# Kernel optimization log

Hardware: AMD Instinct MI355X
Metric: run time of the kernel (lower is better)

Reference implementation:

```python
import jax, jax.numpy as jnp
import numpy as np
jax.config.update("jax_enable_x64", True)

I_SIZE, H, L = 128, 512, 2
B, T = 64, 512


def setup_inputs() -> dict:
    key = jax.random.key(0)
    ks = jax.random.split(key, 9)
    bound = 1.0 / np.sqrt(H)  # PyTorch LSTM init: U(-1/sqrt(H), 1/sqrt(H))
    u = lambda k, shape: jax.random.uniform(k, shape, jnp.float64, -bound, bound)
    return {
        "x": jax.random.normal(ks[0], (B, T, I_SIZE), jnp.float32),
        "W_ih0": u(ks[1], (4 * H, I_SIZE)),
        "W_hh0": u(ks[2], (4 * H, H)),
        "b_ih0": u(ks[3], (4 * H,)),
        "b_hh0": u(ks[4], (4 * H,)),
        "W_ih1": u(ks[5], (4 * H, H)),
        "W_hh1": u(ks[6], (4 * H, H)),
        "b_ih1": u(ks[7], (4 * H,)),
        "b_hh1": u(ks[8], (4 * H,)),
        "h0": jnp.zeros((L, 1, H), jnp.float64),
        "c0": jnp.zeros((L, 1, H), jnp.float64),
    }


def _lstm_layer(x, W_ih, W_hh, b_ih, b_hh, h0, c0):
    # x: [B, T, in]; PyTorch gate order: i, f, g, o
    xg = jnp.einsum("bti,gi->btg", x, W_ih) + b_ih + b_hh  # [B, T, 4H]

    def step(carry, xg_t):
        h, c = carry
        gates = xg_t + h @ W_hh.T  # [B, 4H]
        i, f, g, o = jnp.split(gates, 4, axis=-1)
        c = jax.nn.sigmoid(f) * c + jax.nn.sigmoid(i) * jnp.tanh(g)
        h = jax.nn.sigmoid(o) * jnp.tanh(c)
        return (h, c), h

    (_, _), hs = jax.lax.scan(step, (h0, c0), jnp.swapaxes(xg, 0, 1))
    return jnp.swapaxes(hs, 0, 1)  # [B, T, H]


def reference(x, W_ih0, W_hh0, b_ih0, b_hh0, W_ih1, W_hh1, b_ih1, b_hh1, h0, c0):
    xd = x.astype(jnp.float64)
    b = xd.shape[0]
    h0b = jnp.broadcast_to(h0, (L, b, H))
    c0b = jnp.broadcast_to(c0, (L, b, H))
    out = _lstm_layer(xd, W_ih0, W_hh0, b_ih0, b_hh0, h0b[0], c0b[0])
    out = _lstm_layer(out, W_ih1, W_hh1, b_ih1, b_hh1, h0b[1], c0b[1])
    init_out = jnp.broadcast_to(h0[-1, 0, :], (b, 1, H))
    return jnp.concatenate([init_out, out], axis=1)  # [B, T+1, H]
```

## Files before the change

kernel.cpp:

```cpp
#include <hip/hip_runtime.h>
#include <stdint.h>

typedef _Float16 f16;
typedef _Float16 f16x8 __attribute__((ext_vector_type(8)));
typedef float f32x16 __attribute__((ext_vector_type(16)));
typedef uint32_t u32;
typedef u32 u32x4 __attribute__((ext_vector_type(4)));
typedef u32 u32x2 __attribute__((ext_vector_type(2)));

#define T_ 512

#define SZ_W0  (64u*40u*2048u)
#define SZ_W1  (64u*64u*2048u)
#define OFF_W  0u
#define OFF_X  (SZ_W0 + SZ_W1)
#define SZ_X   (8192u*2048u)
#define OFF_H0 (OFF_X + SZ_X)
#define SZ_HP  (3u*2u*32u*2048u)
#define OFF_H1 (OFF_H0 + SZ_HP)
#define OFF_BIAS (OFF_H1 + SZ_HP)
#define OFF_BAR  (OFF_BIAS + 16384u)
#define WS_NEED  (size_t)(OFF_BAR + 8192u)

#define LDS_ACC  131072
#define LDS_H    (131072 + 4352)
#define LDS_TOTAL (131072 + 4352 + 1280)

__device__ __forceinline__ float sigm(float x) { return 1.0f / (1.0f + __expf(-x)); }
__device__ __forceinline__ float tanh_f(float x) {
  float e = __expf(2.0f * x);
  return 1.0f - 2.0f / (e + 1.0f);
}
__device__ __forceinline__ u32 f16bits(f16 v) {
  return (u32)__builtin_bit_cast(unsigned short, v);
}
__device__ __forceinline__ void store16_llc(void* p, u32x4 v) {
  asm volatile("global_store_dwordx4 %0, %1, off sc0 sc1" :: "v"(p), "v"(v) : "memory");
}
__device__ __forceinline__ void store4_llc(void* p, u32 v) {
  asm volatile("global_store_dword %0, %1, off sc0 sc1" :: "v"(p), "v"(v) : "memory");
}
__device__ __forceinline__ f16x8 load16_llc(const void* p) {
  f16x8 r;
  asm volatile("global_load_dwordx4 %0, %1, off sc0 sc1" : "=v"(r) : "v"(p));
  return r;
}
__device__ __forceinline__ u32x2 load8_llc_wait(const void* p) {
  u32x2 r;
  asm volatile("global_load_dwordx2 %0, %1, off sc0 sc1\n\t"
               "s_waitcnt vmcnt(0)"
               : "=v"(r) : "v"(p) : "memory");
  return r;
}

__global__ void k_packw(const float* __restrict__ Wih0, const float* __restrict__ Whh0,
                        const float* __restrict__ Wih1, const float* __restrict__ Whh1,
                        char* __restrict__ wp) {
  int tid = blockIdx.x * 256 + threadIdx.x;
  int unit = tid >> 6, lane = tid & 63;
  if (unit >= 2560 + 4096) return;
  int layer, hb, ks;
  if (unit < 2560) { layer = 0; hb = unit / 40; ks = unit % 40; }
  else { int u = unit - 2560; layer = 1; hb = u >> 6; ks = u & 63; }
  int col = lane & 31;
  int gate = col >> 3, h8 = col & 7;
  int row = gate * 512 + hb * 8 + h8;
  int khalf = lane >> 5;
  u32 hi[4], lo[4];
#pragma unroll
  for (int jp = 0; jp < 4; ++jp) {
    u32 hv = 0, lv = 0;
#pragma unroll
    for (int e = 0; e < 2; ++e) {
      int j = jp * 2 + e;
      int k = ks * 16 + khalf * 8 + j;
      float w;
      if (layer == 0) w = (k < 128) ? Wih0[row * 128 + k] : Whh0[row * 512 + (k - 128)];
      else            w = (k < 512) ? Wih1[row * 512 + k] : Whh1[row * 512 + (k - 512)];
      f16 h_ = (f16)w; f16 l_ = (f16)(w - (float)h_);
      hv |= f16bits(h_) << (16 * e);
      lv |= f16bits(l_) << (16 * e);
    }
    hi[jp] = hv; lo[jp] = lv;
  }
  char* dst = wp + (layer ? SZ_W0 + (u32)hb * 64u * 2048u : (u32)hb * 40u * 2048u)
                 + (u32)ks * 2048u + (u32)lane * 16u;
  u32x4 vh = {hi[0], hi[1], hi[2], hi[3]};
  u32x4 vl = {lo[0], lo[1], lo[2], lo[3]};
  *(u32x4*)dst = vh;
  *(u32x4*)(dst + 1024) = vl;
}

__global__ void k_packx(const float* __restrict__ x, char* __restrict__ xp) {
  int tid = blockIdx.x * 256 + threadIdx.x;
  int unit = tid >> 6, lane = tid & 63;
  if (unit >= 8192) return;
  int t = unit >> 4, mt = (unit >> 3) & 1, kc = unit & 7;
  int b = mt * 32 + (lane & 31);
  int kbase = kc * 16 + (lane >> 5) * 8;
  const float* src = x + ((size_t)b * T_ + t) * 128 + kbase;
  u32 hi[4], lo[4];
#pragma unroll
  for (int jp = 0; jp < 4; ++jp) {
    u32 hv = 0, lv = 0;
#pragma unroll
    for (int e = 0; e < 2; ++e) {
      float w = src[jp * 2 + e];
      f16 h_ = (f16)w; f16 l_ = (f16)(w - (float)h_);
      hv |= f16bits(h_) << (16 * e);
      lv |= f16bits(l_) << (16 * e);
    }
    hi[jp] = hv; lo[jp] = lv;
  }
  char* dst = xp + (size_t)unit * 2048 + (u32)lane * 16;
  u32x4 vh = {hi[0], hi[1], hi[2], hi[3]};
  u32x4 vl = {lo[0], lo[1], lo[2], lo[3]};
  *(u32x4*)dst = vh;
  *(u32x4*)(dst + 1024) = vl;
}

__global__ void k_init(const float* __restrict__ bih0, const float* __restrict__ bhh0,
                       const float* __restrict__ bih1, const float* __restrict__ bhh1,
                       const float* __restrict__ h0in,
                       float* __restrict__ out, char* __restrict__ ws) {
  int tid = blockIdx.x * 256 + threadIdx.x;
  if (tid < 32768) {
    int b = tid >> 9, h = tid & 511;
    out[(size_t)b * 513 * 512 + h] = h0in[512 + h];
  } else if (tid < 32768 + 8192) {
    int q = tid - 32768; int unit = q >> 6, lane = q & 63;
    int layer = unit >> 6, mt = (unit >> 5) & 1, kc = unit & 31;
    int Hh = kc * 16 + (lane >> 5) * 8;
    u32 hi[4], lo[4];
#pragma unroll
    for (int jp = 0; jp < 4; ++jp) {
      u32 hv = 0, lv = 0;
#pragma unroll
      for (int e = 0; e < 2; ++e) {
        float w = h0in[layer * 512 + Hh + jp * 2 + e];
        f16 h_ = (f16)w; f16 l_ = (f16)(w - (float)h_);
        hv |= f16bits(h_) << (16 * e);
        lv |= f16bits(l_) << (16 * e);
      }
      hi[jp] = hv; lo[jp] = lv;
    }
    int buf = layer ? 0 : 2;
    char* dst = ws + (layer ? OFF_H1 : OFF_H0)
                   + ((u32)(buf * 2 + mt) * 32 + (u32)kc) * 2048u + (u32)lane * 16u;
    u32x4 vh = {hi[0], hi[1], hi[2], hi[3]};
    u32x4 vl = {lo[0], lo[1], lo[2], lo[3]};
    *(u32x4*)dst = vh;
    *(u32x4*)(dst + 1024) = vl;
  } else if (tid < 32768 + 8192 + 4096) {
    int j = tid - 40960; int layer = j >> 11, jj = j & 2047;
    const float* a = layer ? bih1 : bih0;
    const float* b2 = layer ? bhh1 : bhh0;
    ((float*)(ws + OFF_BIAS))[layer * 2048 + jj] = a[jj] + b2[jj];
  } else if (tid < 45056 + 256) {
    int g = tid - 45056; int mt = g >> 7, idx = g & 127;
    *(u32*)(ws + OFF_BAR + (u32)mt * 4096u + (u32)idx * 4u) = 0u;
  }
}

#define ISSUE_BLOCK(AH, AL, bb) \
  _Pragma("unroll") for (int i_ = 0; i_ < 8; ++i_) { \
    AH[i_] = load16_llc((bb) + (u32)i_ * 2048u + lo16); \
    AL[i_] = load16_llc((bb) + (u32)i_ * 2048u + 1024u + lo16); }

#define MFMA_BLOCK(AH, AL, BLK) \
  _Pragma("unroll") for (int i_ = 0; i_ < 8; ++i_) { \
    f16x8 bhi_ = *(const f16x8*)(smem + (u32)((BLK) * 8 + i_) * 2048u + lo16); \
    f16x8 blo_ = *(const f16x8*)(smem + (u32)((BLK) * 8 + i_) * 2048u + 1024u + lo16); \
    accA = __builtin_amdgcn_mfma_f32_32x32x16_f16(AH[i_], bhi_, accA, 0, 0, 0); \
    accB = __builtin_amdgcn_mfma_f32_32x32x16_f16(AH[i_], blo_, accB, 0, 0, 0); \
    accC = __builtin_amdgcn_mfma_f32_32x32x16_f16(AL[i_], bhi_, accC, 0, 0, 0); }

#define BBASE(B) ((B) < splitblk ? a0 + (u32)(B) * 16384u : a1 + (u32)((B) - splitblk) * 16384u)

__global__ __launch_bounds__(64, 1)
void k_main(char* ws, const float* c0in, float* __restrict__ out) {
  extern __shared__ char smem[];
  const int wg = blockIdx.x;
  const int mt = wg & 1, layer = (wg >> 1) & 1, hb = wg >> 2;
  const int lane = threadIdx.x;
  const int nk = layer ? 64 : 40;
  const int nb = layer ? 8 : 5;
  const int splitblk = layer ? 4 : 1;

  {
    const char* wsrc = ws + OFF_W + (layer ? SZ_W0 + (u32)hb * 64u * 2048u : (u32)hb * 40u * 2048u);
    int nbytes = nk * 2048;
    for (int off = lane * 16; off < nbytes; off += 1024)
      *(u32x4*)(smem + off) = *(const u32x4*)(wsrc + off);
  }
  float* accS = (float*)(smem + LDS_ACC);
  float* hS   = (float*)(smem + LDS_H);
  const float* bias = (const float*)(ws + OFF_BIAS) + layer * 2048;
  const int hl = lane & 7, rg = lane >> 3;
  const int Hid = hb * 8 + hl;
  const float bi = bias[0 * 512 + Hid], bf = bias[1 * 512 + Hid];
  const float bg = bias[2 * 512 + Hid], bo = bias[3 * 512 + Hid];
  float c[4];
  { float ci = c0in[layer * 512 + Hid]; c[0] = c[1] = c[2] = c[3] = ci; }
  u32* flags = (u32*)(ws + OFF_BAR + (u32)mt * 4096u);
  const u32* myflagp = flags + (u32)lane * 2u;
  u32* myslot = flags + ((u32)layer * 64u + (u32)hb);
  const u32 tgt_sub = (lane >= 32 && layer == 0) ? 1u : 0u;
  const char* xp  = ws + OFF_X;
  const char* h0p = ws + OFF_H0;
  const char* h1p = ws + OFF_H1;
  const u32 lo16 = (u32)lane * 16u;
  f16x8 Ah0[8], Al0[8], Ah1[8], Al1[8];
  __syncthreads();

  for (int s = 0; s <= T_; ++s) {
    const bool active = layer ? (s >= 1) : (s < T_);
    if (active) {
      const int t = layer ? (s - 1) : s;
      const int rbuf = (s + 2) % 3, wbuf = s % 3;
      const char* a0; const char* a1;
      if (layer == 0) {
        a0 = xp + (u32)(t * 2 + mt) * 8u * 2048u;
        a1 = h0p + ((u32)(rbuf * 2 + mt) * 32u) * 2048u;
      } else {
        a0 = h0p + ((u32)(rbuf * 2 + mt) * 32u) * 2048u;
        a1 = h1p + ((u32)(rbuf * 2 + mt) * 32u) * 2048u;
      }
      f32x16 accA = {}, accB = {}, accC = {};
      ISSUE_BLOCK(Ah0, Al0, BBASE(0));
#pragma unroll
      for (int blk = 0; blk < 8; blk += 2) if (blk < nb) {
        if (blk + 1 < nb) { ISSUE_BLOCK(Ah1, Al1, BBASE(blk + 1));
                            asm volatile("s_waitcnt vmcnt(16)" ::: "memory"); }
        else              { asm volatile("s_waitcnt vmcnt(0)" ::: "memory"); }
        __builtin_amdgcn_sched_barrier(0);
        MFMA_BLOCK(Ah0, Al0, blk);
        if (blk + 1 < nb) {
          if (blk + 2 < nb) { ISSUE_BLOCK(Ah0, Al0, BBASE(blk + 2));
                              asm volatile("s_waitcnt vmcnt(16)" ::: "memory"); }
          else              { asm volatile("s_waitcnt vmcnt(0)" ::: "memory"); }
          __builtin_amdgcn_sched_barrier(0);
          MFMA_BLOCK(Ah1, Al1, blk + 1);
        }
      }
#pragma unroll
      for (int r = 0; r < 16; ++r) {
        int row = (r & 3) + 8 * (r >> 2) + 4 * (lane >> 5);
        accS[row * 33 + (lane & 31)] = accA[r] + accB[r] + accC[r];
      }
      __syncthreads();
      float* outp = out + (size_t)(mt * 32) * 513 * 512 + (size_t)(t + 1) * 512 + Hid;
#pragma unroll
      for (int j = 0; j < 4; ++j) {
        int row = rg * 4 + j;
        float gi = accS[row * 33 + hl] + bi;
        float gf = accS[row * 33 + 8 + hl] + bf;
        float gg = accS[row * 33 + 16 + hl] + bg;
        float go = accS[row * 33 + 24 + hl] + bo;
        float iv = sigm(gi), fv = sigm(gf), gv = tanh_f(gg), ov = sigm(go);
        float cc = fv * c[j] + iv * gv; c[j] = cc;
        float hv = ov * tanh_f(cc);
        hS[row * 9 + hl] = hv;
        if (layer) outp[(size_t)row * 513 * 512] = hv;
      }
      __syncthreads();
      if ((lane >> 5) == (hb & 1)) {
        int r32 = lane & 31;
        u32 hi[4], lo[4];
#pragma unroll
        for (int jp = 0; jp < 4; ++jp) {
          float v0 = hS[r32 * 9 + jp * 2], v1 = hS[r32 * 9 + jp * 2 + 1];
          f16 a_ = (f16)v0; f16 b_ = (f16)(v0 - (float)a_);
          f16 c_ = (f16)v1; f16 d_ = (f16)(v1 - (float)c_);
          hi[jp] = f16bits(a_) | (f16bits(c_) << 16);
          lo[jp] = f16bits(b_) | (f16bits(d_) << 16);
        }
        char* dst = (char*)(layer ? h1p : h0p)
                  + ((u32)(wbuf * 2 + mt) * 32 + (u32)(hb >> 1)) * 2048u + lo16;
        u32x4 vh = {hi[0], hi[1], hi[2], hi[3]};
        u32x4 vl = {lo[0], lo[1], lo[2], lo[3]};
        store16_llc(dst, vh);
        store16_llc(dst + 1024, vl);
      }
    }
    if (s < T_) {
      asm volatile("s_waitcnt vmcnt(0)" ::: "memory");
      if (lane == 0) store4_llc(myslot, (u32)(s + 1));
      const u32 tgt = (u32)(s + 1) - tgt_sub;
      for (;;) {
        u32x2 v = load8_llc_wait(myflagp);
        __builtin_amdgcn_sched_barrier(0);
        if (__all((v.x >= tgt) && (v.y >= tgt))) break;
        __builtin_amdgcn_s_sleep(1);
      }
      __builtin_amdgcn_sched_barrier(0);
      asm volatile("" ::: "memory");
    }
  }
}

extern "C" void kernel_launch(void* const* d_in, const int* in_sizes, int n_in,
                              void* d_out, int out_size, void* d_ws, size_t ws_size,
                              hipStream_t stream) {
  const float* x    = (const float*)d_in[0];
  const float* Wih0 = (const float*)d_in[1];
  const float* Whh0 = (const float*)d_in[2];
  const float* bih0 = (const float*)d_in[3];
  const float* bhh0 = (const float*)d_in[4];
  const float* Wih1 = (const float*)d_in[5];
  const float* Whh1 = (const float*)d_in[6];
  const float* bih1 = (const float*)d_in[7];
  const float* bhh1 = (const float*)d_in[8];
  const float* h0   = (const float*)d_in[9];
  const float* c0   = (const float*)d_in[10];
  float* out = (float*)d_out;
  char* ws = (char*)d_ws;
  if (ws_size < WS_NEED) return;

  hipFuncSetAttribute((const void*)k_main,
                      hipFuncAttributeMaxDynamicSharedMemorySize, LDS_TOTAL);

  k_packw<<<1664, 256, 0, stream>>>(Wih0, Whh0, Wih1, Whh1, ws + OFF_W);
  k_packx<<<2048, 256, 0, stream>>>(x, ws + OFF_X);
  k_init<<<177, 256, 0, stream>>>(bih0, bhh0, bih1, bhh1, h0, out, ws);
  k_main<<<256, 64, LDS_TOTAL, stream>>>(ws, c0, out);
}
```

Baseline: 4.566 ms.

## Split per-step K reduction across four waves with LDS partial-sum reduction

Each workgroup grows from one wave to four. The K dimension of the per-step MFMA GEMM is split across the waves, with 10 or 16 k-slices per wave. Partial accumulators go to separate LDS regions and are summed during the gate computation, where each thread now handles one row. This shortens the serial per-step latency of loading and running the MFMA chain, at the cost of more LDS traffic and a larger workgroup in the latency-bound recurrent loop.

```diff
diff --git a/kernel.cpp b/kernel.cpp
--- a/kernel.cpp
+++ b/kernel.cpp
@@ -23,8 +23,8 @@
 #define WS_NEED  (size_t)(OFF_BAR + 8192u)
 
 #define LDS_ACC  131072
-#define LDS_H    (131072 + 4352)
-#define LDS_TOTAL (131072 + 4352 + 1280)
+#define LDS_H    (131072 + 16896)
+#define LDS_TOTAL (131072 + 16896 + 1152)
 
 __device__ __forceinline__ float sigm(float x) { return 1.0f / (1.0f + __expf(-x)); }
 __device__ __forceinline__ float tanh_f(float x) {
@@ -162,55 +162,81 @@
   }
 }
 
-#define ISSUE_BLOCK(AH, AL, bb) \
-  _Pragma("unroll") for (int i_ = 0; i_ < 8; ++i_) { \
-    AH[i_] = load16_llc((bb) + (u32)i_ * 2048u + lo16); \
-    AL[i_] = load16_llc((bb) + (u32)i_ * 2048u + 1024u + lo16); }
-
-#define MFMA_BLOCK(AH, AL, BLK) \
-  _Pragma("unroll") for (int i_ = 0; i_ < 8; ++i_) { \
-    f16x8 bhi_ = *(const f16x8*)(smem + (u32)((BLK) * 8 + i_) * 2048u + lo16); \
-    f16x8 blo_ = *(const f16x8*)(smem + (u32)((BLK) * 8 + i_) * 2048u + 1024u + lo16); \
-    accA = __builtin_amdgcn_mfma_f32_32x32x16_f16(AH[i_], bhi_, accA, 0, 0, 0); \
-    accB = __builtin_amdgcn_mfma_f32_32x32x16_f16(AH[i_], blo_, accB, 0, 0, 0); \
-    accC = __builtin_amdgcn_mfma_f32_32x32x16_f16(AL[i_], bhi_, accC, 0, 0, 0); }
-
-#define BBASE(B) ((B) < splitblk ? a0 + (u32)(B) * 16384u : a1 + (u32)((B) - splitblk) * 16384u)
-
-__global__ __launch_bounds__(64, 1)
+template<int LKS, int SPLITKS>
+__device__ __forceinline__ void k_step_mfma(const char* a0, const char* a1,
+                                            const char* smem, int k0, u32 lo16,
+                                            f32x16& accA, f32x16& accB, f32x16& accC) {
+  f16x8 Ah[LKS], Al[LKS];
+#pragma unroll
+  for (int i = 0; i < LKS; ++i) {
+    int ks = k0 + i;
+    const char* ab = (ks < SPLITKS) ? (a0 + (u32)ks * 2048u)
+                                    : (a1 + (u32)(ks - SPLITKS) * 2048u);
+    Ah[i] = load16_llc(ab + lo16);
+    Al[i] = load16_llc(ab + 1024u + lo16);
+  }
+  constexpr int C1 = (LKS > 8) ? 8 : LKS;
+  constexpr int W1 = 2 * (LKS - C1);
+  if constexpr (W1 == 16)     asm volatile("s_waitcnt vmcnt(16)" ::: "memory");
+  else if constexpr (W1 == 4) asm volatile("s_waitcnt vmcnt(4)" ::: "memory");
+  else                        asm volatile("s_waitcnt vmcnt(0)" ::: "memory");
+  __builtin_amdgcn_sched_barrier(0);
+#pragma unroll
+  for (int i = 0; i < C1; ++i) {
+    f16x8 bhi = *(const f16x8*)(smem + (u32)(k0 + i) * 2048u + lo16);
+    f16x8 blo = *(const f16x8*)(smem + (u32)(k0 + i) * 2048u + 1024u + lo16);
+    accA = __builtin_amdgcn_mfma_f32_32x32x16_f16(Ah[i], bhi, accA, 0, 0, 0);
+    accB = __builtin_amdgcn_mfma_f32_32x32x16_f16(Ah[i], blo, accB, 0, 0, 0);
+    accC = __builtin_amdgcn_mfma_f32_32x32x16_f16(Al[i], bhi, accC, 0, 0, 0);
+  }
+  if constexpr (LKS > C1) {
+    asm volatile("s_waitcnt vmcnt(0)" ::: "memory");
+    __builtin_amdgcn_sched_barrier(0);
+#pragma unroll
+    for (int i = C1; i < LKS; ++i) {
+      f16x8 bhi = *(const f16x8*)(smem + (u32)(k0 + i) * 2048u + lo16);
+      f16x8 blo = *(const f16x8*)(smem + (u32)(k0 + i) * 2048u + 1024u + lo16);
+      accA = __builtin_amdgcn_mfma_f32_32x32x16_f16(Ah[i], bhi, accA, 0, 0, 0);
+      accB = __builtin_amdgcn_mfma_f32_32x32x16_f16(Ah[i], blo, accB, 0, 0, 0);
+      accC = __builtin_amdgcn_mfma_f32_32x32x16_f16(Al[i], bhi, accC, 0, 0, 0);
+    }
+  }
+}
+
+__global__ __launch_bounds__(256, 1)
 void k_main(char* ws, const float* c0in, float* __restrict__ out) {
   extern __shared__ char smem[];
   const int wg = blockIdx.x;
   const int mt = wg & 1, layer = (wg >> 1) & 1, hb = wg >> 2;
-  const int lane = threadIdx.x;
+  const int tid = threadIdx.x;
+  const int l = tid & 63;
+  const int wv = tid >> 6;
   const int nk = layer ? 64 : 40;
-  const int nb = layer ? 8 : 5;
-  const int splitblk = layer ? 4 : 1;
 
   {
     const char* wsrc = ws + OFF_W + (layer ? SZ_W0 + (u32)hb * 64u * 2048u : (u32)hb * 40u * 2048u);
     int nbytes = nk * 2048;
-    for (int off = lane * 16; off < nbytes; off += 1024)
+    for (int off = tid * 16; off < nbytes; off += 4096)
       *(u32x4*)(smem + off) = *(const u32x4*)(wsrc + off);
   }
-  float* accS = (float*)(smem + LDS_ACC);
+  float* accP = (float*)(smem + LDS_ACC);
   float* hS   = (float*)(smem + LDS_H);
   const float* bias = (const float*)(ws + OFF_BIAS) + layer * 2048;
-  const int hl = lane & 7, rg = lane >> 3;
+  const int hl = tid & 7;
+  const int rloc = wv * 8 + ((tid >> 3) & 7);
   const int Hid = hb * 8 + hl;
   const float bi = bias[0 * 512 + Hid], bf = bias[1 * 512 + Hid];
   const float bg = bias[2 * 512 + Hid], bo = bias[3 * 512 + Hid];
-  float c[4];
-  { float ci = c0in[layer * 512 + Hid]; c[0] = c[1] = c[2] = c[3] = ci; }
+  float c = c0in[layer * 512 + Hid];
   u32* flags = (u32*)(ws + OFF_BAR + (u32)mt * 4096u);
-  const u32* myflagp = flags + (u32)lane * 2u;
+  const u32* myflagp = flags + (u32)l * 2u;
   u32* myslot = flags + ((u32)layer * 64u + (u32)hb);
-  const u32 tgt_sub = (lane >= 32 && layer == 0) ? 1u : 0u;
+  const u32 tgt_sub = (l >= 32 && layer == 0) ? 1u : 0u;
   const char* xp  = ws + OFF_X;
   const char* h0p = ws + OFF_H0;
   const char* h1p = ws + OFF_H1;
-  const u32 lo16 = (u32)lane * 16u;
-  f16x8 Ah0[8], Al0[8], Ah1[8], Al1[8];
+  const u32 lo16 = (u32)l * 16u;
+  const int k0 = wv * (layer ? 16 : 10);
   __syncthreads();
 
   for (int s = 0; s <= T_; ++s) {
@@ -227,45 +253,34 @@
         a1 = h1p + ((u32)(rbuf * 2 + mt) * 32u) * 2048u;
       }
       f32x16 accA = {}, accB = {}, accC = {};
-      ISSUE_BLOCK(Ah0, Al0, BBASE(0));
-#pragma unroll
-      for (int blk = 0; blk < 8; blk += 2) if (blk < nb) {
-        if (blk + 1 < nb) { ISSUE_BLOCK(Ah1, Al1, BBASE(blk + 1));
-                            asm volatile("s_waitcnt vmcnt(16)" ::: "memory"); }
-        else              { asm volatile("s_waitcnt vmcnt(0)" ::: "memory"); }
-        __builtin_amdgcn_sched_barrier(0);
-        MFMA_BLOCK(Ah0, Al0, blk);
-        if (blk + 1 < nb) {
-          if (blk + 2 < nb) { ISSUE_BLOCK(Ah0, Al0, BBASE(blk + 2));
-                              asm volatile("s_waitcnt vmcnt(16)" ::: "memory"); }
-          else              { asm volatile("s_waitcnt vmcnt(0)" ::: "memory"); }
-          __builtin_amdgcn_sched_barrier(0);
-          MFMA_BLOCK(Ah1, Al1, blk + 1);
+      if (layer == 0) k_step_mfma<10, 8 >(a0, a1, smem, k0, lo16, accA, accB, accC);
+      else            k_step_mfma<16, 32>(a0, a1, smem, k0, lo16, accA, accB, accC);
+      {
+        float* ap = accP + wv * 1056;
+#pragma unroll
+        for (int r = 0; r < 16; ++r) {
+          int row = (r & 3) + 8 * (r >> 2) + 4 * (l >> 5);
+          ap[row * 33 + (l & 31)] = accA[r] + accB[r] + accC[r];
         }
       }
-#pragma unroll
-      for (int r = 0; r < 16; ++r) {
-        int row = (r & 3) + 8 * (r >> 2) + 4 * (lane >> 5);
-        accS[row * 33 + (lane & 31)] = accA[r] + accB[r] + accC[r];
-      }
       __syncthreads();
-      float* outp = out + (size_t)(mt * 32) * 513 * 512 + (size_t)(t + 1) * 512 + Hid;
-#pragma unroll
-      for (int j = 0; j < 4; ++j) {
-        int row = rg * 4 + j;
-        float gi = accS[row * 33 + hl] + bi;
-        float gf = accS[row * 33 + 8 + hl] + bf;
-        float gg = accS[row * 33 + 16 + hl] + bg;
-        float go = accS[row * 33 + 24 + hl] + bo;
+      {
+        float gi = bi, gf = bf, gg = bg, go = bo;
+#pragma unroll
+        for (int p = 0; p < 4; ++p) {
+          const float* ap = accP + p * 1056 + rloc * 33;
+          gi += ap[hl]; gf += ap[8 + hl]; gg += ap[16 + hl]; go += ap[24 + hl];
+        }
         float iv = sigm(gi), fv = sigm(gf), gv = tanh_f(gg), ov = sigm(go);
-        float cc = fv * c[j] + iv * gv; c[j] = cc;
-        float hv = ov * tanh_f(cc);
-        hS[row * 9 + hl] = hv;
-        if (layer) outp[(size_t)row * 513 * 512] = hv;
+        c = fv * c + iv * gv;
+        float hv = ov * tanh_f(c);
+        hS[rloc * 9 + hl] = hv;
+        if (layer)
+          out[(size_t)(mt * 32 + rloc) * 513 * 512 + (size_t)(t + 1) * 512 + Hid] = hv;
       }
       __syncthreads();
-      if ((lane >> 5) == (hb & 1)) {
-        int r32 = lane & 31;
+      if (wv == 0 && (l >> 5) == (hb & 1)) {
+        int r32 = l & 31;
         u32 hi[4], lo[4];
 #pragma unroll
         for (int jp = 0; jp < 4; ++jp) {
@@ -285,7 +300,7 @@
     }
     if (s < T_) {
       asm volatile("s_waitcnt vmcnt(0)" ::: "memory");
-      if (lane == 0) store4_llc(myslot, (u32)(s + 1));
+      if (tid == 0) store4_llc(myslot, (u32)(s + 1));
       const u32 tgt = (u32)(s + 1) - tgt_sub;
       for (;;) {
         u32x2 v = load8_llc_wait(myflagp);
@@ -323,5 +338,5 @@
   k_packw<<<1664, 256, 0, stream>>>(Wih0, Whh0, Wih1, Whh1, ws + OFF_W);
   k_packx<<<2048, 256, 0, stream>>>(x, ws + OFF_X);
   k_init<<<177, 256, 0, stream>>>(bih0, bhh0, bih1, bhh1, h0, out, ws);
-  k_main<<<256, 64, LDS_TOTAL, stream>>>(ws, c0, out);
-}
+  k_main<<<256, 256, LDS_TOTAL, stream>>>(ws, c0, out);
+}
```

After: 4.008 ms. -12.2%, faster.
